# Kernel optimization log

Measured on AMD Instinct MI355X. Metric: run time of the kernel, lower is better.

The kernel has to match this reference:

```python
import jax, jax.numpy as jnp
import numpy as np

B, TK, H = 32, 8192, 256

def setup_inputs() -> dict:
    key = jax.random.key(0)
    ks = jax.random.split(key, 10)
    s = 0.02
    return {
        "s_t_hat": jax.random.normal(ks[0], (B, 2 * H), dtype=jnp.float32),
        "encoder_outputs": jax.random.normal(ks[1], (B, TK, H), dtype=jnp.float32),
        "enc_padding_mask": jnp.ones((B, TK), dtype=jnp.float32),
        "coverage": jax.random.uniform(ks[2], (B, TK), dtype=jnp.float32),
        "attn_dist_node_to_token": jax.random.uniform(ks[3], (B, TK), dtype=jnp.float32),
        "We": jax.random.normal(ks[4], (H, H), dtype=jnp.float32) * s,   # encode_proj weight
        "Wd": jax.random.normal(ks[5], (H, 2 * H), dtype=jnp.float32) * s,  # decode_proj weight
        "bd": jax.random.normal(ks[6], (H,), dtype=jnp.float32) * s,     # decode_proj bias
        "wc": jax.random.normal(ks[7], (H,), dtype=jnp.float32) * s,     # W_c weight (Linear(1,H))
        "v": jax.random.normal(ks[8], (H,), dtype=jnp.float32) * s,      # v weight (Linear(H,1))
    }

def reference(s_t_hat, encoder_outputs, enc_padding_mask, coverage,
              attn_dist_node_to_token, We, Wd, bd, wc, v):
    # encoder projection: [b,t,h] @ We^T -> [b,t,h]
    enc_feat = jnp.einsum('bth,gh->btg', encoder_outputs, We)
    # decoder projection: [b,2h] @ Wd^T + bd -> [b,h]
    dec_fea = s_t_hat @ Wd.T + bd
    # coverage feature: outer product coverage[b,t] x wc[h]
    att_features = enc_feat + dec_fea[:, None, :] + coverage[..., None] * wc
    e = jnp.tanh(att_features)
    scores = jnp.einsum('bth,h->bt', e, v)  # [b, t_k]
    attn_ = jax.nn.softmax(scores, axis=1) * enc_padding_mask
    attn = attn_ / jnp.sum(attn_, axis=1, keepdims=True)
    c_t = jnp.einsum('bt,bth->bh', attn, encoder_outputs)  # context
    new_cov = jnp.clip(coverage + attn, 0.0, 1.0)
    return (c_t, attn, new_cov)
```

## Files before the change

kernel.cpp:

```cpp
#include <hip/hip_runtime.h>

#define B_  32
#define TK_ 8192
#define H_  256
#define MT  64
#define NT  4

typedef __bf16 bf16_t;
typedef __bf16 bf16x4 __attribute__((ext_vector_type(4)));
typedef __bf16 bf16x8 __attribute__((ext_vector_type(8)));
typedef float  floatx4 __attribute__((ext_vector_type(4)));

__device__ __forceinline__ float tanh_fast(float x) {
    float e = __builtin_amdgcn_exp2f(x * 2.885390081777927f);
    return 1.0f - 2.0f * __builtin_amdgcn_rcpf(e + 1.0f);
}

__global__ void prep_kernel(const float* __restrict__ s_t_hat,
                            const float* __restrict__ We,
                            const float* __restrict__ Wd,
                            const float* __restrict__ bd,
                            bf16_t* __restrict__ We_bf,
                            float* __restrict__ dec_ws,
                            float* __restrict__ D_ws) {
    int tid = threadIdx.x, blk = blockIdx.x;
    int gid = blk * 256 + tid;
    We_bf[gid] = (bf16_t)We[gid];

    if (gid < 32) D_ws[gid] = 0.f;

    if (blk >= 32 && blk < 160) {
        int idx  = (blk - 32) * 256 + tid;
        int pair = idx >> 2, q = idx & 3;
        int b = pair >> 8, i = pair & 255;
        const float4* sp = (const float4*)(s_t_hat + b * 2 * H_ + q * 128);
        const float4* wp = (const float4*)(Wd + (size_t)i * 2 * H_ + q * 128);
        float sum = 0.f;
        #pragma unroll 8
        for (int ii = 0; ii < 32; ++ii) {
            float4 a = sp[ii], w = wp[ii];
            sum += a.x * w.x + a.y * w.y + a.z * w.z + a.w * w.w;
        }
        sum += __shfl_xor(sum, 1, 64);
        sum += __shfl_xor(sum, 2, 64);
        if (q == 0) dec_ws[pair] = sum + bd[i];
    }
}

__global__ __launch_bounds__(256, 4) void attn_main(
    const float* __restrict__ enc,
    const float* __restrict__ mask,
    const float* __restrict__ cov,
    const float* __restrict__ wc,
    const float* __restrict__ v,
    const bf16_t* __restrict__ We_bf,
    const float* __restrict__ dec_ws,
    float* __restrict__ ctx_part,
    float* __restrict__ D_ws,
    float* __restrict__ attn_out) {

    __shared__ __align__(16) bf16_t As[MT * 264];
    __shared__ float dec_s[256], wc_s[256], v_s[256];
    __shared__ float cov_s[64], mask_s[64];
    __shared__ float sp[4][64];
    __shared__ float ctx_acc[256];

    const int tid  = threadIdx.x;
    const int b    = blockIdx.y;
    const int lane = tid & 63, w = tid >> 6;
    const int l15  = lane & 15, l4 = lane >> 4;
    const int h4   = lane * 4;
    const int wbase = w * 64;
    const int kf = l4 * 8;
    const bf16_t* Bp = We_bf + (size_t)wbase * 256;

    dec_s[tid] = dec_ws[b * 256 + tid];
    wc_s[tid]  = wc[tid];
    v_s[tid]   = v[tid];
    ctx_acc[tid] = 0.f;

    float dsum = 0.f;

    for (int it4 = 0; it4 < NT; ++it4) {
        const int t0 = (blockIdx.x * NT + it4) * MT;

        if (tid < 64)       cov_s[tid]       = cov[(size_t)b * TK_ + t0 + tid];
        else if (tid < 128) mask_s[tid - 64] = mask[(size_t)b * TK_ + t0 + tid - 64];

        const float* encb = enc + ((size_t)b * TK_ + t0) * H_;
        {
            float4 r[8];
            #pragma unroll
            for (int it = 0; it < 8; ++it)
                r[it] = *(const float4*)(encb + (size_t)(it * 4 + w) * H_ + h4);
            #pragma unroll
            for (int it = 0; it < 8; ++it) {
                bf16x4 p;
                p[0] = (bf16_t)r[it].x; p[1] = (bf16_t)r[it].y;
                p[2] = (bf16_t)r[it].z; p[3] = (bf16_t)r[it].w;
                *(bf16x4*)(&As[(it * 4 + w) * 264 + h4]) = p;
            }
            #pragma unroll
            for (int it = 0; it < 8; ++it)
                r[it] = *(const float4*)(encb + (size_t)((it + 8) * 4 + w) * H_ + h4);
            #pragma unroll
            for (int it = 0; it < 8; ++it) {
                bf16x4 p;
                p[0] = (bf16_t)r[it].x; p[1] = (bf16_t)r[it].y;
                p[2] = (bf16_t)r[it].z; p[3] = (bf16_t)r[it].w;
                *(bf16x4*)(&As[((it + 8) * 4 + w) * 264 + h4]) = p;
            }
        }
        __syncthreads();

        floatx4 acc[4][4];
        #pragma unroll
        for (int mi = 0; mi < 4; ++mi)
            #pragma unroll
            for (int ni = 0; ni < 4; ++ni)
                acc[mi][ni] = (floatx4){0.f, 0.f, 0.f, 0.f};

        bf16x8 bq[4];
        #pragma unroll
        for (int ni = 0; ni < 4; ++ni)
            bq[ni] = *(const bf16x8*)(Bp + (size_t)(ni * 16 + l15) * 256 + kf);

        #pragma unroll
        for (int ks = 0; ks < 8; ++ks) {
            bf16x8 bqn[4];
            if (ks < 7) {
                int kn = (ks + 1) * 32 + kf;
                #pragma unroll
                for (int ni = 0; ni < 4; ++ni)
                    bqn[ni] = *(const bf16x8*)(Bp + (size_t)(ni * 16 + l15) * 256 + kn);
            }
            int k = ks * 32 + kf;
            bf16x8 a[4];
            #pragma unroll
            for (int mi = 0; mi < 4; ++mi)
                a[mi] = *(const bf16x8*)(&As[(mi * 16 + l15) * 264 + k]);
            #pragma unroll
            for (int mi = 0; mi < 4; ++mi)
                #pragma unroll
                for (int ni = 0; ni < 4; ++ni)
                    acc[mi][ni] = __builtin_amdgcn_mfma_f32_16x16x32_bf16(
                        a[mi], bq[ni], acc[mi][ni], 0, 0, 0);
            if (ks < 7) {
                #pragma unroll
                for (int ni = 0; ni < 4; ++ni)
                    bq[ni] = bqn[ni];
            }
        }

        float decv[4], wcv[4], vv[4];
        #pragma unroll
        for (int ni = 0; ni < 4; ++ni) {
            int g = wbase + ni * 16 + l15;
            decv[ni] = dec_s[g]; wcv[ni] = wc_s[g]; vv[ni] = v_s[g];
        }
        #pragma unroll
        for (int mi = 0; mi < 4; ++mi) {
            #pragma unroll
            for (int r = 0; r < 4; ++r) {
                int t = mi * 16 + l4 * 4 + r;
                float cv = cov_s[t];
                float s = 0.f;
                #pragma unroll
                for (int ni = 0; ni < 4; ++ni) {
                    float af = acc[mi][ni][r] + decv[ni] + cv * wcv[ni];
                    s += tanh_fast(af) * vv[ni];
                }
                s += __shfl_xor(s, 1, 64);
                s += __shfl_xor(s, 2, 64);
                s += __shfl_xor(s, 4, 64);
                s += __shfl_xor(s, 8, 64);
                if (l15 == 0) sp[w][t] = s;
            }
        }
        __syncthreads();

        float sc = sp[0][lane] + sp[1][lane] + sp[2][lane] + sp[3][lane];
        float wv = __builtin_amdgcn_exp2f(sc * 1.4426950408889634f) * mask_s[lane];

        if (w == 0) {
            attn_out[(size_t)b * TK_ + t0 + lane] = wv;
            float d = wv;
            d += __shfl_xor(d, 1, 64);  d += __shfl_xor(d, 2, 64);
            d += __shfl_xor(d, 4, 64);  d += __shfl_xor(d, 8, 64);
            d += __shfl_xor(d, 16, 64); d += __shfl_xor(d, 32, 64);
            dsum += d;
        }

        {
            float c0 = 0, c1 = 0, c2 = 0, c3 = 0;
            #pragma unroll
            for (int tt = 0; tt < 16; ++tt) {
                int t = w * 16 + tt;
                float wvt = __shfl(wv, t, 64);
                bf16x4 q = *(const bf16x4*)(&As[t * 264 + h4]);
                c0 += wvt * (float)q[0];
                c1 += wvt * (float)q[1];
                c2 += wvt * (float)q[2];
                c3 += wvt * (float)q[3];
            }
            atomicAdd(&ctx_acc[h4 + 0], c0);
            atomicAdd(&ctx_acc[h4 + 1], c1);
            atomicAdd(&ctx_acc[h4 + 2], c2);
            atomicAdd(&ctx_acc[h4 + 3], c3);
        }
        __syncthreads();
    }

    if (tid == 0) atomicAdd(&D_ws[b], dsum);
    ctx_part[((size_t)b * 32 + blockIdx.x) * 256 + tid] = ctx_acc[tid];
}

__global__ void finalize_kernel(const float* __restrict__ cov,
                                const float* __restrict__ ctx_part,
                                const float* __restrict__ D_ws,
                                float* __restrict__ out) {
    int b = blockIdx.y, chunk = blockIdx.x, tid = threadIdx.x;
    float invD = 1.0f / D_ws[b];
    int idx = chunk * 256 + tid;
    size_t gi = (size_t)b * TK_ + idx;
    float* attn = out + 8192;
    float* ncov = out + 8192 + (size_t)B_ * TK_;
    float a = attn[gi] * invD;
    attn[gi] = a;
    float nc = cov[gi] + a;
    ncov[gi] = fminf(fmaxf(nc, 0.f), 1.f);
    if (chunk == 0) {
        const float* p = ctx_part + (size_t)b * 32 * 256 + tid;
        float s0 = 0, s1 = 0, s2 = 0, s3 = 0;
        #pragma unroll
        for (int j = 0; j < 32; j += 4) {
            s0 += p[(j + 0) * 256];
            s1 += p[(j + 1) * 256];
            s2 += p[(j + 2) * 256];
            s3 += p[(j + 3) * 256];
        }
        out[b * 256 + tid] = ((s0 + s1) + (s2 + s3)) * invD;
    }
}

extern "C" void kernel_launch(void* const* d_in, const int* in_sizes, int n_in,
                              void* d_out, int out_size, void* d_ws, size_t ws_size,
                              hipStream_t stream) {
    const float* s_t_hat = (const float*)d_in[0];
    const float* enc     = (const float*)d_in[1];
    const float* mask    = (const float*)d_in[2];
    const float* cov     = (const float*)d_in[3];
    const float* We      = (const float*)d_in[5];
    const float* Wd      = (const float*)d_in[6];
    const float* bd      = (const float*)d_in[7];
    const float* wc      = (const float*)d_in[8];
    const float* v       = (const float*)d_in[9];
    float* out = (float*)d_out;

    char* ws = (char*)d_ws;
    bf16_t* We_bf  = (bf16_t*)ws;
    float*  dec_ws = (float*)(ws + 131072);
    float*  D_ws   = (float*)(ws + 131072 + 32768);
    float*  ctx_part = (float*)(ws + 196608);

    prep_kernel<<<256, 256, 0, stream>>>(s_t_hat, We, Wd, bd, We_bf, dec_ws, D_ws);
    attn_main<<<dim3(32, 32), 256, 0, stream>>>(enc, mask, cov, wc, v, We_bf,
                                                dec_ws, ctx_part, D_ws, out + 8192);
    finalize_kernel<<<dim3(32, 32), 256, 0, stream>>>(cov, ctx_part, D_ws, out);
}
```

Measured before the change: 499.7 us.

## Halve tile size, double grid, and prefetch next encoder tile into registers

Shrinks the per-iteration token tile from 64 to 32 and doubles the grid to 64x32 blocks. The next tile's encoder rows are loaded into registers while the current tile runs its MFMA and softmax work, so global loads overlap compute. Context partial sums now stay in registers across iterations and go through shared-memory atomics once per block instead of once per tile. Batch order is reversed and launch bounds are relaxed to 3 waves per EU, which may affect occupancy, and the finalize step must now reduce twice as many partials.

```diff
diff --git a/kernel.cpp b/kernel.cpp
--- a/kernel.cpp
+++ b/kernel.cpp
@@ -3,7 +3,7 @@
 #define B_  32
 #define TK_ 8192
 #define H_  256
-#define MT  64
+#define MT  32
 #define NT  4
 
 typedef __bf16 bf16_t;
@@ -47,7 +47,7 @@
     }
 }
 
-__global__ __launch_bounds__(256, 4) void attn_main(
+__global__ __launch_bounds__(256, 3) void attn_main(
     const float* __restrict__ enc,
     const float* __restrict__ mask,
     const float* __restrict__ cov,
@@ -61,12 +61,12 @@
 
     __shared__ __align__(16) bf16_t As[MT * 264];
     __shared__ float dec_s[256], wc_s[256], v_s[256];
-    __shared__ float cov_s[64], mask_s[64];
-    __shared__ float sp[4][64];
+    __shared__ float cov_s[MT], mask_s[MT];
+    __shared__ float sp[4][MT];
     __shared__ float ctx_acc[256];
 
     const int tid  = threadIdx.x;
-    const int b    = blockIdx.y;
+    const int b    = 31 - blockIdx.y;
     const int lane = tid & 63, w = tid >> 6;
     const int l15  = lane & 15, l4 = lane >> 4;
     const int h4   = lane * 4;
@@ -74,48 +74,47 @@
     const int kf = l4 * 8;
     const bf16_t* Bp = We_bf + (size_t)wbase * 256;
 
+    const size_t tbase = (size_t)b * TK_ + (size_t)blockIdx.x * (NT * MT);
+    const float* encb0 = enc + tbase * H_;
+
+    float4 r[8];
+    #pragma unroll
+    for (int it = 0; it < 8; ++it)
+        r[it] = *(const float4*)(encb0 + (size_t)(it * 4 + w) * H_ + h4);
+
     dec_s[tid] = dec_ws[b * 256 + tid];
     wc_s[tid]  = wc[tid];
     v_s[tid]   = v[tid];
     ctx_acc[tid] = 0.f;
 
     float dsum = 0.f;
-
-    for (int it4 = 0; it4 < NT; ++it4) {
-        const int t0 = (blockIdx.x * NT + it4) * MT;
-
-        if (tid < 64)       cov_s[tid]       = cov[(size_t)b * TK_ + t0 + tid];
-        else if (tid < 128) mask_s[tid - 64] = mask[(size_t)b * TK_ + t0 + tid - 64];
-
-        const float* encb = enc + ((size_t)b * TK_ + t0) * H_;
-        {
-            float4 r[8];
+    float c0 = 0.f, c1 = 0.f, c2 = 0.f, c3 = 0.f;
+
+    for (int t4 = 0; t4 < NT; ++t4) {
+        const int t0 = t4 * MT;
+
+        if (tid < MT)           cov_s[tid]       = cov[tbase + t0 + tid];
+        else if (tid < 2 * MT)  mask_s[tid - MT] = mask[tbase + t0 + tid - MT];
+
+        #pragma unroll
+        for (int it = 0; it < 8; ++it) {
+            bf16x4 p;
+            p[0] = (bf16_t)r[it].x; p[1] = (bf16_t)r[it].y;
+            p[2] = (bf16_t)r[it].z; p[3] = (bf16_t)r[it].w;
+            *(bf16x4*)(&As[(it * 4 + w) * 264 + h4]) = p;
+        }
+        __syncthreads();
+
+        if (t4 + 1 < NT) {
+            const float* encn = encb0 + (size_t)(t0 + MT) * H_;
             #pragma unroll
             for (int it = 0; it < 8; ++it)
-                r[it] = *(const float4*)(encb + (size_t)(it * 4 + w) * H_ + h4);
-            #pragma unroll
-            for (int it = 0; it < 8; ++it) {
-                bf16x4 p;
-                p[0] = (bf16_t)r[it].x; p[1] = (bf16_t)r[it].y;
-                p[2] = (bf16_t)r[it].z; p[3] = (bf16_t)r[it].w;
-                *(bf16x4*)(&As[(it * 4 + w) * 264 + h4]) = p;
-            }
-            #pragma unroll
-            for (int it = 0; it < 8; ++it)
-                r[it] = *(const float4*)(encb + (size_t)((it + 8) * 4 + w) * H_ + h4);
-            #pragma unroll
-            for (int it = 0; it < 8; ++it) {
-                bf16x4 p;
-                p[0] = (bf16_t)r[it].x; p[1] = (bf16_t)r[it].y;
-                p[2] = (bf16_t)r[it].z; p[3] = (bf16_t)r[it].w;
-                *(bf16x4*)(&As[((it + 8) * 4 + w) * 264 + h4]) = p;
-            }
-        }
-        __syncthreads();
-
-        floatx4 acc[4][4];
-        #pragma unroll
-        for (int mi = 0; mi < 4; ++mi)
+                r[it] = *(const float4*)(encn + (size_t)(it * 4 + w) * H_ + h4);
+        }
+
+        floatx4 acc[2][4];
+        #pragma unroll
+        for (int mi = 0; mi < 2; ++mi)
             #pragma unroll
             for (int ni = 0; ni < 4; ++ni)
                 acc[mi][ni] = (floatx4){0.f, 0.f, 0.f, 0.f};
@@ -135,12 +134,12 @@
                     bqn[ni] = *(const bf16x8*)(Bp + (size_t)(ni * 16 + l15) * 256 + kn);
             }
             int k = ks * 32 + kf;
-            bf16x8 a[4];
-            #pragma unroll
-            for (int mi = 0; mi < 4; ++mi)
+            bf16x8 a[2];
+            #pragma unroll
+            for (int mi = 0; mi < 2; ++mi)
                 a[mi] = *(const bf16x8*)(&As[(mi * 16 + l15) * 264 + k]);
             #pragma unroll
-            for (int mi = 0; mi < 4; ++mi)
+            for (int mi = 0; mi < 2; ++mi)
                 #pragma unroll
                 for (int ni = 0; ni < 4; ++ni)
                     acc[mi][ni] = __builtin_amdgcn_mfma_f32_16x16x32_bf16(
@@ -159,15 +158,15 @@
             decv[ni] = dec_s[g]; wcv[ni] = wc_s[g]; vv[ni] = v_s[g];
         }
         #pragma unroll
-        for (int mi = 0; mi < 4; ++mi) {
-            #pragma unroll
-            for (int r = 0; r < 4; ++r) {
-                int t = mi * 16 + l4 * 4 + r;
+        for (int mi = 0; mi < 2; ++mi) {
+            #pragma unroll
+            for (int rr = 0; rr < 4; ++rr) {
+                int t = mi * 16 + l4 * 4 + rr;
                 float cv = cov_s[t];
                 float s = 0.f;
                 #pragma unroll
                 for (int ni = 0; ni < 4; ++ni) {
-                    float af = acc[mi][ni][r] + decv[ni] + cv * wcv[ni];
+                    float af = acc[mi][ni][rr] + decv[ni] + cv * wcv[ni];
                     s += tanh_fast(af) * vv[ni];
                 }
                 s += __shfl_xor(s, 1, 64);
@@ -179,40 +178,39 @@
         }
         __syncthreads();
 
-        float sc = sp[0][lane] + sp[1][lane] + sp[2][lane] + sp[3][lane];
-        float wv = __builtin_amdgcn_exp2f(sc * 1.4426950408889634f) * mask_s[lane];
+        int tl = lane & 31;
+        float sc = sp[0][tl] + sp[1][tl] + sp[2][tl] + sp[3][tl];
+        float wv = __builtin_amdgcn_exp2f(sc * 1.4426950408889634f) * mask_s[tl];
 
         if (w == 0) {
-            attn_out[(size_t)b * TK_ + t0 + lane] = wv;
+            if (lane < 32) attn_out[tbase + t0 + lane] = wv;
             float d = wv;
             d += __shfl_xor(d, 1, 64);  d += __shfl_xor(d, 2, 64);
             d += __shfl_xor(d, 4, 64);  d += __shfl_xor(d, 8, 64);
-            d += __shfl_xor(d, 16, 64); d += __shfl_xor(d, 32, 64);
-            dsum += d;
-        }
-
-        {
-            float c0 = 0, c1 = 0, c2 = 0, c3 = 0;
-            #pragma unroll
-            for (int tt = 0; tt < 16; ++tt) {
-                int t = w * 16 + tt;
-                float wvt = __shfl(wv, t, 64);
-                bf16x4 q = *(const bf16x4*)(&As[t * 264 + h4]);
-                c0 += wvt * (float)q[0];
-                c1 += wvt * (float)q[1];
-                c2 += wvt * (float)q[2];
-                c3 += wvt * (float)q[3];
-            }
-            atomicAdd(&ctx_acc[h4 + 0], c0);
-            atomicAdd(&ctx_acc[h4 + 1], c1);
-            atomicAdd(&ctx_acc[h4 + 2], c2);
-            atomicAdd(&ctx_acc[h4 + 3], c3);
+            d += __shfl_xor(d, 16, 64);
+            if (lane == 0) dsum += d;
+        }
+
+        #pragma unroll
+        for (int tt = 0; tt < 8; ++tt) {
+            int t = w * 8 + tt;
+            float wvt = __shfl(wv, t, 64);
+            bf16x4 q = *(const bf16x4*)(&As[t * 264 + h4]);
+            c0 += wvt * (float)q[0];
+            c1 += wvt * (float)q[1];
+            c2 += wvt * (float)q[2];
+            c3 += wvt * (float)q[3];
         }
         __syncthreads();
     }
 
     if (tid == 0) atomicAdd(&D_ws[b], dsum);
-    ctx_part[((size_t)b * 32 + blockIdx.x) * 256 + tid] = ctx_acc[tid];
+    atomicAdd(&ctx_acc[h4 + 0], c0);
+    atomicAdd(&ctx_acc[h4 + 1], c1);
+    atomicAdd(&ctx_acc[h4 + 2], c2);
+    atomicAdd(&ctx_acc[h4 + 3], c3);
+    __syncthreads();
+    ctx_part[((size_t)b * 64 + blockIdx.x) * 256 + tid] = ctx_acc[tid];
 }
 
 __global__ void finalize_kernel(const float* __restrict__ cov,
@@ -230,10 +228,10 @@
     float nc = cov[gi] + a;
     ncov[gi] = fminf(fmaxf(nc, 0.f), 1.f);
     if (chunk == 0) {
-        const float* p = ctx_part + (size_t)b * 32 * 256 + tid;
+        const float* p = ctx_part + (size_t)b * 64 * 256 + tid;
         float s0 = 0, s1 = 0, s2 = 0, s3 = 0;
         #pragma unroll
-        for (int j = 0; j < 32; j += 4) {
+        for (int j = 0; j < 64; j += 4) {
             s0 += p[(j + 0) * 256];
             s1 += p[(j + 1) * 256];
             s2 += p[(j + 2) * 256];
@@ -264,7 +262,7 @@
     float*  ctx_part = (float*)(ws + 196608);
 
     prep_kernel<<<256, 256, 0, stream>>>(s_t_hat, We, Wd, bd, We_bf, dec_ws, D_ws);
-    attn_main<<<dim3(32, 32), 256, 0, stream>>>(enc, mask, cov, wc, v, We_bf,
+    attn_main<<<dim3(64, 32), 256, 0, stream>>>(enc, mask, cov, wc, v, We_bf,
                                                 dec_ws, ctx_part, D_ws, out + 8192);
     finalize_kernel<<<dim3(32, 32), 256, 0, stream>>>(cov, ctx_part, D_ws, out);
 }
```

Measured after the change: 611.7 us. +22.4%, slower.
